# Kernel optimization log

Measured on AMD Instinct MI355X. Metric: run time of the kernel, lower is better.

## Reference

```python
import jax, jax.numpy as jnp
import numpy as np

NB, NC, NT = 64, 128, 6
NEURON = (25, 50, 100)
AXIS = 4
EPS = 1e-12


def _offdiag_idx(nc):
    # static [nc, nc-1] column indices of the off-diagonal entries per row
    idx = np.tile(np.arange(nc)[None, :], (nc, 1))
    mask = ~np.eye(nc, dtype=bool)
    return idx[mask].reshape(nc, nc - 1)


def setup_inputs() -> dict:
    key = jax.random.key(0)
    ks = jax.random.split(key, 8)
    P = NT * NT
    coords = jax.random.normal(ks[0], (NB, NC, 3), dtype=jnp.float32)
    atom_types = jax.random.randint(ks[1], (NC,), 0, NT)
    dims = [1] + list(NEURON)
    inp = {"coords": coords, "atom_types": atom_types}
    for i in range(3):
        bound = 1.0 / float(np.sqrt(dims[i]))
        inp[f"W{i+1}"] = jax.random.uniform(ks[2 + 2 * i], (P, dims[i + 1], dims[i]), jnp.float32, -bound, bound)
        inp[f"b{i+1}"] = jax.random.uniform(ks[3 + 2 * i], (P, dims[i + 1]), jnp.float32, -bound, bound)
    return inp


def _channel_dense(x, W, b, channels, res_mode):
    # x: [nb, Ppairs, in]; W[channels]: [Ppairs, out, in] (redundant per-pair gather, as in torch)
    y = jnp.einsum('bpi,poi->bpo', x, W[channels]) + b[channels]
    y = jnp.tanh(y)
    if res_mode == 1:
        y = y + x
    elif res_mode == 2:
        y = y + jnp.concatenate([x, x], axis=-1)
    return y


def _forward(coords, atom_types, W1, b1, W2, b2, W3, b3):
    nb, nc, _ = coords.shape
    idx = jnp.asarray(_offdiag_idx(nc))  # [nc, nc-1], static
    row = jnp.arange(nc)[:, None]

    rij = coords[:, :, None, :] - coords[:, None, :, :]          # [nb,nc,nc,3]
    rij = rij[:, row, idx]                                       # [nb,nc,nc-1,3] off-diagonal
    dij = jnp.linalg.norm(rij, axis=-1)                          # [nb,nc,nc-1]
    dinv = 1.0 / jnp.maximum(dij, EPS)
    loc_env_r = dinv
    loc_env_a = rij * (dinv * dinv)[..., None]                   # [nb,nc,nc-1,3]

    neighbor_types = atom_types[idx]                             # [nc,nc-1]
    channels = (atom_types[:, None] * NT + neighbor_types).reshape(-1)  # [nc*(nc-1)]

    x = loc_env_r.reshape(nb, -1, 1)                             # [nb,P,1]
    y = _channel_dense(x, W1, b1, channels, res_mode=0)          # 1 -> 25
    y = _channel_dense(y, W2, b2, channels, res_mode=2)          # 25 -> 50 (+concat res)
    y = _channel_dense(y, W3, b3, channels, res_mode=2)          # 50 -> 100 (+concat res)

    out = y.reshape(nb, nc, nc - 1, NEURON[-1])                  # [nb,nc,k,100]
    t1 = jnp.einsum('bnka,bnkf->bnaf', loc_env_a, out[..., :AXIS])   # [nb,nc,3,4]
    t2 = jnp.einsum('bnka,bnaf->bnkf', loc_env_a, t1)                # [nb,nc,k,4]
    res = jnp.einsum('bnkg,bnkf->bngf', out, t2)                     # [nb,nc,100,4]
    return res.reshape(nb, nc, -1)


def reference(coords, atom_types, W1, b1, W2, b2, W3, b3):
    return _forward(coords, atom_types, W1, b1, W2, b2, W3, b3)
```

## Files before the change

### kernel.cpp

```cpp
#include <hip/hip_runtime.h>

#define NBATCH 64
#define NCH    128
#define NTYPE  6
#define NK     127
#define N1     25
#define N2     50
#define N3     100
#define NAXIS  4
#define OUTPER 400
#define W2P    28
#define W3P4   52
#define MAXKP  152
#define MAXC4  38

#define R4(M)  M(0) M(1) M(2) M(3)
#define R5(M)  M(0) M(1) M(2) M(3) M(4)
#define R7(M)  M(0) M(1) M(2) M(3) M(4) M(5) M(6)
#define R12(M) M(0) M(1) M(2) M(3) M(4) M(5) M(6) M(7) M(8) M(9) M(10) M(11)
#define R25(M) M(0) M(1) M(2) M(3) M(4) M(5) M(6) M(7) M(8) M(9) M(10) M(11) M(12) \
               M(13) M(14) M(15) M(16) M(17) M(18) M(19) M(20) M(21) M(22) M(23) M(24)
#define R50(M) R25(M) M(25) M(26) M(27) M(28) M(29) M(30) M(31) M(32) M(33) M(34) \
               M(35) M(36) M(37) M(38) M(39) M(40) M(41) M(42) M(43) M(44) M(45) \
               M(46) M(47) M(48) M(49)

__device__ __forceinline__ float tanh_fast(float x) {
    float e = __expf(2.0f * x);
    return 1.0f - 2.0f * __builtin_amdgcn_rcpf(e + 1.0f);
}

__global__ void k_transpose(const float* __restrict__ coords, float* __restrict__ ct) {
    int t = blockIdx.x * blockDim.x + threadIdx.x;
    if (t >= NBATCH * NCH * 3) return;
    int b  = t & (NBATCH - 1);
    int jd = t >> 6;
    int d  = jd % 3;
    int j  = jd / 3;
    ct[t] = coords[(b * NCH + j) * 3 + d];
}

__device__ __forceinline__ void sort_pad(
    const int* __restrict__ types, int n, int* tysh, int* ksp, int* chs, int* aux,
    int tid, int nthr)
{
    for (int t = tid; t < NCH; t += nthr) tysh[t] = types[t];
    __syncthreads();
    if (tid == 0) {
        int cnt[NTYPE], pos[NTYPE];
        for (int t = 0; t < NTYPE; ++t) cnt[t] = 0;
        for (int k = 0; k < NK; ++k) { int j = (k < n) ? k : k + 1; cnt[tysh[j]]++; }
        int c = 0;
        for (int t = 0; t < NTYPE; ++t) {
            pos[t] = c;
            int pc = (cnt[t] + 3) & ~3;
            for (int q = c >> 2; q < (c + pc) >> 2; ++q) chs[q] = t;
            for (int p = c + cnt[t]; p < c + pc; ++p) ksp[p] = -1;
            c += pc;
        }
        aux[0] = c >> 2;
        for (int k = 0; k < NK; ++k) { int j = (k < n) ? k : k + 1; ksp[pos[tysh[j]]++] = k; }
    }
    __syncthreads();
}

__global__ __launch_bounds__(256, 4) void k_mlp(
    const float* __restrict__ ct, const int* __restrict__ types,
    const float* __restrict__ W1, const float* __restrict__ B1,
    const float* __restrict__ W2, const float* __restrict__ B2,
    const float* __restrict__ W3, const float* __restrict__ B3,
    float* __restrict__ t1buf)
{
    __shared__ float w2s[N2 * W2P];
    __shared__ float w3s4[4 * W3P4];
    __shared__ float w1s[N1], b1s[N1], b2s[N2], b3s4[4];
    __shared__ int   ksp[MAXKP];
    __shared__ int   chs[MAXC4];
    __shared__ int   tysh[NCH];
    __shared__ int   aux[1];

    const int n   = blockIdx.x >> 2;
    const int qc  = blockIdx.x & 3;
    const int w   = threadIdx.x >> 6;
    const int b   = threadIdx.x & 63;
    const int tid = threadIdx.x;

    sort_pad(types, n, tysh, ksp, chs, aux, tid, 256);
    const int nch4 = __builtin_amdgcn_readfirstlane(aux[0]);
    const int c_lo = (qc * nch4) >> 2;
    const int c_hi = ((qc + 1) * nch4) >> 2;

    const int tn = __builtin_amdgcn_readfirstlane(tysh[n]);
    const float cx = ct[(n*3+0)*NBATCH + b];
    const float cy = ct[(n*3+1)*NBATCH + b];
    const float cz = ct[(n*3+2)*NBATCH + b];

    float t1a[12];
#define TIN(i) t1a[i] = 0.0f;
    R12(TIN)
#undef TIN

    int prevty = -1;
    for (int kc = c_lo; kc < c_hi; ++kc) {
        const int tj = __builtin_amdgcn_readfirstlane(chs[kc]);
        const int ch = tn * NTYPE + tj;
        if (tj != prevty) {
            __syncthreads();
            for (int idx = tid; idx < N2*N1; idx += 256)
                w2s[(idx / N1) * W2P + (idx % N1)] = W2[ch*(N2*N1) + idx];
            for (int idx = tid; idx < 4*N2; idx += 256)
                w3s4[(idx / N2) * W3P4 + (idx % N2)] = W3[ch*(N3*N2) + idx];
            if (tid < N1) { w1s[tid] = W1[ch*N1+tid]; b1s[tid] = B1[ch*N1+tid]; }
            if (tid < N2) b2s[tid] = B2[ch*N2+tid];
            if (tid < 4)  b3s4[tid] = B3[ch*N3+tid];
            prevty = tj;
            __syncthreads();
        }
        const int sk = __builtin_amdgcn_readfirstlane(ksp[kc*4 + w]);
        if (sk < 0) continue;
        const int j = (sk < n) ? sk : sk + 1;

        const float dx = cx - ct[(j*3+0)*NBATCH + b];
        const float dy = cy - ct[(j*3+1)*NBATCH + b];
        const float dz = cz - ct[(j*3+2)*NBATCH + b];
        const float d2 = dx*dx + dy*dy + dz*dz;
        const float dd = sqrtf(d2);
        const float dinv = __builtin_amdgcn_rcpf(fmaxf(dd, 1e-12f));
        const float di2 = dinv * dinv;
        const float ax = dx * di2, ay = dy * di2, az = dz * di2;

        float y1[N1];
#define L1S(o) y1[o] = tanh_fast(fmaf(dinv, w1s[o], b1s[o]));
        R25(L1S)
#undef L1S

        float zf0 = b3s4[0], zf1 = b3s4[1], zf2 = b3s4[2], zf3 = b3s4[3];
        float r[4];
#define P1Q(o,q) { float4 wq = *(const float4*)&w2s[(o)*W2P + (q)*4]; \
                   z = fmaf(wq.x, y1[(q)*4+0], z); z = fmaf(wq.y, y1[(q)*4+1], z); \
                   z = fmaf(wq.z, y1[(q)*4+2], z); z = fmaf(wq.w, y1[(q)*4+3], z); }
#define MLP2(o) { float z = b2s[o]; \
                  P1Q(o,0) P1Q(o,1) P1Q(o,2) P1Q(o,3) P1Q(o,4) P1Q(o,5) \
                  z = fmaf(w2s[(o)*W2P + 24], y1[24], z); \
                  float y2o = tanh_fast(z) + y1[(o)%N1]; \
                  if ((o) < 4) r[(o)&3] = y2o; \
                  zf0 = fmaf(w3s4[0*W3P4+(o)], y2o, zf0); \
                  zf1 = fmaf(w3s4[1*W3P4+(o)], y2o, zf1); \
                  zf2 = fmaf(w3s4[2*W3P4+(o)], y2o, zf2); \
                  zf3 = fmaf(w3s4[3*W3P4+(o)], y2o, zf3); }
        R50(MLP2)
#undef MLP2
#undef P1Q

#define O4F(f) { float o4 = tanh_fast(f==0?zf0:f==1?zf1:f==2?zf2:zf3) + r[f]; \
        t1a[0+(f)] = fmaf(ax, o4, t1a[0+(f)]); \
        t1a[4+(f)] = fmaf(ay, o4, t1a[4+(f)]); \
        t1a[8+(f)] = fmaf(az, o4, t1a[8+(f)]); }
        O4F(0) O4F(1) O4F(2) O4F(3)
#undef O4F
    }

    float* dst = t1buf + (n * 12) * NBATCH + b;
#define TAT(i) atomicAdd(dst + (i) * NBATCH, t1a[i]);
    R12(TAT)
#undef TAT
}

__global__ __launch_bounds__(1024, 8) void k_res2(
    const float* __restrict__ ct, const int* __restrict__ types,
    const float* __restrict__ W1, const float* __restrict__ B1,
    const float* __restrict__ W2, const float* __restrict__ B2,
    const float* __restrict__ W3, const float* __restrict__ B3,
    const float* __restrict__ t1buf, float* __restrict__ out)
{
    __shared__ float y2t[4 * N2 * NBATCH];
    __shared__ float t2s[4 * NBATCH * NAXIS];
    __shared__ float w2s[N2 * W2P];
    __shared__ float w1s[N1], b1s[N1], b2s[N2];
    __shared__ int   ksp[MAXKP];
    __shared__ int   chs[MAXC4];
    __shared__ int   tysh[NCH];
    __shared__ int   aux[1];

    const int n    = blockIdx.x >> 1;
    const int kh   = blockIdx.x & 1;
    const int w    = threadIdx.x >> 6;
    const int lane = threadIdx.x & 63;
    const int kk2  = w >> 1;
    const int h    = w & 1;
    const int tid  = threadIdx.x;

    sort_pad(types, n, tysh, ksp, chs, aux, tid, 1024);
    const int nch4 = __builtin_amdgcn_readfirstlane(aux[0]);
    const int c_lo = kh ? (nch4 >> 1) : 0;
    const int c_hi = kh ? nch4 : (nch4 >> 1);

    const int tn = __builtin_amdgcn_readfirstlane(tysh[n]);

    float t1r[12];
#define T1L(i) t1r[i] = t1buf[(n*12 + (i))*NBATCH + lane];
    R12(T1L)
#undef T1L

    const int g0 = __builtin_amdgcn_readfirstlane(w * 7);
    int gg[7], rr[7];
#define GGI(gi) gg[gi] = ((g0 + (gi)) < N3) ? (g0 + (gi)) : (N3 - 1); \
                rr[gi] = (gg[gi] >= N2) ? (gg[gi] - N2) : gg[gi];
    R7(GGI)
#undef GGI

    float racc[7][4];
#define RIN(gi) racc[gi][0]=0.f; racc[gi][1]=0.f; racc[gi][2]=0.f; racc[gi][3]=0.f;
    R7(RIN)
#undef RIN

    float b3v[7];
    int prevty = -1;

    for (int kc = c_lo; kc < c_hi; ++kc) {
        const int tj = __builtin_amdgcn_readfirstlane(chs[kc]);
        const int ch = tn * NTYPE + tj;
        if (tj != prevty) {
            for (int idx = tid; idx < N2*N1; idx += 1024)
                w2s[(idx / N1) * W2P + (idx % N1)] = W2[ch*(N2*N1) + idx];
            if (tid < N1) { w1s[tid] = W1[ch*N1+tid]; b1s[tid] = B1[ch*N1+tid]; }
            if (tid < N2) b2s[tid] = B2[ch*N2+tid];
#define B3L(gi) b3v[gi] = B3[ch*N3 + gg[gi]];
            R7(B3L)
#undef B3L
            prevty = tj;
            __syncthreads();
        }
        const int kb = kc * 4;
        if (w < 8) {
            const int sk = __builtin_amdgcn_readfirstlane(ksp[kb + kk2]);
            if (sk >= 0) {
                const int j = (sk < n) ? sk : sk + 1;
                const float dx = ct[(n*3+0)*NBATCH + lane] - ct[(j*3+0)*NBATCH + lane];
                const float dy = ct[(n*3+1)*NBATCH + lane] - ct[(j*3+1)*NBATCH + lane];
                const float dz = ct[(n*3+2)*NBATCH + lane] - ct[(j*3+2)*NBATCH + lane];
                const float d2 = dx*dx + dy*dy + dz*dz;
                const float dd = sqrtf(d2);
                const float dinv = __builtin_amdgcn_rcpf(fmaxf(dd, 1e-12f));

                if (h == 0) {
                    const float di2 = dinv * dinv;
                    const float ax = dx * di2, ay = dy * di2, az = dz * di2;
#define T2W(f) t2s[(kk2*NBATCH + lane)*NAXIS + (f)] = \
                    ax*t1r[f] + ay*t1r[4+(f)] + az*t1r[8+(f)];
                    T2W(0) T2W(1) T2W(2) T2W(3)
#undef T2W
                }

                float y1[N1];
#define L1S(o) y1[o] = tanh_fast(fmaf(dinv, w1s[o], b1s[o]));
                R25(L1S)
#undef L1S
                const int ob = h * N1;
                float* y2w = &y2t[(kk2*N2 + ob)*NBATCH + lane];
#define P1Q(oi,q) { float4 wq = *(const float4*)&w2s[(ob+(oi))*W2P + (q)*4]; \
                    z = fmaf(wq.x, y1[(q)*4+0], z); z = fmaf(wq.y, y1[(q)*4+1], z); \
                    z = fmaf(wq.z, y1[(q)*4+2], z); z = fmaf(wq.w, y1[(q)*4+3], z); }
#define P1S(oi) { float z = b2s[ob+(oi)]; \
                  P1Q(oi,0) P1Q(oi,1) P1Q(oi,2) P1Q(oi,3) P1Q(oi,4) P1Q(oi,5) \
                  z = fmaf(w2s[(ob+(oi))*W2P + 24], y1[24], z); \
                  y2w[(oi)*NBATCH] = tanh_fast(z) + y1[oi]; }
                R25(P1S)
#undef P1S
#undef P1Q
            }
        }
        __syncthreads();
        const float* w3b = W3 + ch * (N3*N2);
        for (int kp = 0; kp < 2; ++kp) {
            const int skA = __builtin_amdgcn_readfirstlane(ksp[kb + kp*2 + 0]);
            const int skB = __builtin_amdgcn_readfirstlane(ksp[kb + kp*2 + 1]);
            if (skA < 0 && skB < 0) continue;
            const float* y2A = &y2t[((kp*2+0)*N2)*NBATCH + lane];
            const float* y2B = &y2t[((kp*2+1)*N2)*NBATCH + lane];
            float zA[7], zB[7];
#define ZIN(gi) zA[gi] = b3v[gi]; zB[gi] = b3v[gi];
            R7(ZIN)
#undef ZIN
            for (int ic = 0; ic < 10; ++ic) {
                const int io = ic * 5;
                float w35[7][5];
#define W35L(gi) w35[gi][0]=w3b[gg[gi]*N2+io+0]; w35[gi][1]=w3b[gg[gi]*N2+io+1]; \
                 w35[gi][2]=w3b[gg[gi]*N2+io+2]; w35[gi][3]=w3b[gg[gi]*N2+io+3]; \
                 w35[gi][4]=w3b[gg[gi]*N2+io+4];
                R7(W35L)
#undef W35L
                if (skA >= 0) {
                    float yv[5];
#define LDA(i) yv[i] = y2A[(io + (i))*NBATCH];
                    R5(LDA)
#undef LDA
#define FA(gi) zA[gi]=fmaf(w35[gi][0],yv[0],zA[gi]); zA[gi]=fmaf(w35[gi][1],yv[1],zA[gi]); \
               zA[gi]=fmaf(w35[gi][2],yv[2],zA[gi]); zA[gi]=fmaf(w35[gi][3],yv[3],zA[gi]); \
               zA[gi]=fmaf(w35[gi][4],yv[4],zA[gi]);
                    R7(FA)
#undef FA
                }
                if (skB >= 0) {
                    float yv[5];
#define LDB(i) yv[i] = y2B[(io + (i))*NBATCH];
                    R5(LDB)
#undef LDB
#define FB(gi) zB[gi]=fmaf(w35[gi][0],yv[0],zB[gi]); zB[gi]=fmaf(w35[gi][1],yv[1],zB[gi]); \
               zB[gi]=fmaf(w35[gi][2],yv[2],zB[gi]); zB[gi]=fmaf(w35[gi][3],yv[3],zB[gi]); \
               zB[gi]=fmaf(w35[gi][4],yv[4],zB[gi]);
                    R7(FB)
#undef FB
                }
            }
            if (skA >= 0) {
                const float4 t2v = *(const float4*)&t2s[((kp*2+0)*NBATCH + lane)*NAXIS];
#define PFA(gi) { float o3 = tanh_fast(zA[gi]) + y2A[rr[gi]*NBATCH]; \
                  racc[gi][0] = fmaf(o3, t2v.x, racc[gi][0]); \
                  racc[gi][1] = fmaf(o3, t2v.y, racc[gi][1]); \
                  racc[gi][2] = fmaf(o3, t2v.z, racc[gi][2]); \
                  racc[gi][3] = fmaf(o3, t2v.w, racc[gi][3]); }
                R7(PFA)
#undef PFA
            }
            if (skB >= 0) {
                const float4 t2v = *(const float4*)&t2s[((kp*2+1)*NBATCH + lane)*NAXIS];
#define PFB(gi) { float o3 = tanh_fast(zB[gi]) + y2B[rr[gi]*NBATCH]; \
                  racc[gi][0] = fmaf(o3, t2v.x, racc[gi][0]); \
                  racc[gi][1] = fmaf(o3, t2v.y, racc[gi][1]); \
                  racc[gi][2] = fmaf(o3, t2v.z, racc[gi][2]); \
                  racc[gi][3] = fmaf(o3, t2v.w, racc[gi][3]); }
                R7(PFB)
#undef PFB
            }
        }
        __syncthreads();
    }

#define PST(gi) if (g0 + (gi) < N3) { \
        float* dp = &out[(lane*NCH + n)*OUTPER + gg[gi]*NAXIS]; \
        atomicAdd(dp + 0, racc[gi][0]); \
        atomicAdd(dp + 1, racc[gi][1]); \
        atomicAdd(dp + 2, racc[gi][2]); \
        atomicAdd(dp + 3, racc[gi][3]); }
    R7(PST)
#undef PST
}

extern "C" void kernel_launch(void* const* d_in, const int* in_sizes, int n_in,
                              void* d_out, int out_size, void* d_ws, size_t ws_size,
                              hipStream_t stream) {
    const float* coords = (const float*)d_in[0];
    const int*   types  = (const int*)d_in[1];
    const float* W1 = (const float*)d_in[2];
    const float* B1 = (const float*)d_in[3];
    const float* W2 = (const float*)d_in[4];
    const float* B2 = (const float*)d_in[5];
    const float* W3 = (const float*)d_in[6];
    const float* B3 = (const float*)d_in[7];
    float* out = (float*)d_out;

    float* t1buf = (float*)d_ws;
    float* ct    = t1buf + NCH * 12 * NBATCH;

    hipMemsetAsync(t1buf, 0, (size_t)NCH * 12 * NBATCH * sizeof(float), stream);
    hipMemsetAsync(out, 0, (size_t)out_size * sizeof(float), stream);

    k_transpose<<<(NBATCH*NCH*3 + 255)/256, 256, 0, stream>>>(coords, ct);
    k_mlp <<<NCH*4, 256, 0, stream>>>(ct, types, W1,B1,W2,B2,W3,B3, t1buf);
    k_res2<<<NCH*2, 1024, 0, stream>>>(ct, types, W1,B1,W2,B2,W3,B3, t1buf, out);
}
```

Baseline: 1.013 ms.

## Split k_res2 output features across blocks, drop LDS weight staging, use row-major y2

k_res2 now launches 4 blocks per atom of 512 threads each. The extra block dimension splits the 100 output features into two halves of 50, so each wave owns 7 features within its half. W1/W2/B1/B2 are read straight from global memory, which removes the LDS staging and the per-type-change barrier. The y2 intermediate moves to a per-lane row-major layout with padded rows so it can be read and written as float4, and absent neighbours are zero-filled so the skip branches go away. The cost is that layer 1 and layer 2 are recomputed in both feature-half blocks, and padded neighbours now do work they previously skipped.

```diff
diff --git a/kernel.cpp b/kernel.cpp
--- a/kernel.cpp
+++ b/kernel.cpp
@@ -11,15 +11,20 @@
 #define OUTPER 400
 #define W2P    28
 #define W3P4   52
+#define Y2ROW  28
 #define MAXKP  152
 #define MAXC4  38
 
 #define R4(M)  M(0) M(1) M(2) M(3)
 #define R5(M)  M(0) M(1) M(2) M(3) M(4)
+#define R6(M)  M(0) M(1) M(2) M(3) M(4) M(5)
 #define R7(M)  M(0) M(1) M(2) M(3) M(4) M(5) M(6)
 #define R12(M) M(0) M(1) M(2) M(3) M(4) M(5) M(6) M(7) M(8) M(9) M(10) M(11)
 #define R25(M) M(0) M(1) M(2) M(3) M(4) M(5) M(6) M(7) M(8) M(9) M(10) M(11) M(12) \
                M(13) M(14) M(15) M(16) M(17) M(18) M(19) M(20) M(21) M(22) M(23) M(24)
+#define R25A(M,a) M(a,0) M(a,1) M(a,2) M(a,3) M(a,4) M(a,5) M(a,6) M(a,7) M(a,8) M(a,9) \
+               M(a,10) M(a,11) M(a,12) M(a,13) M(a,14) M(a,15) M(a,16) M(a,17) M(a,18) \
+               M(a,19) M(a,20) M(a,21) M(a,22) M(a,23) M(a,24)
 #define R50(M) R25(M) M(25) M(26) M(27) M(28) M(29) M(30) M(31) M(32) M(33) M(34) \
                M(35) M(36) M(37) M(38) M(39) M(40) M(41) M(42) M(43) M(44) M(45) \
                M(46) M(47) M(48) M(49)
@@ -165,23 +170,22 @@
 #undef TAT
 }
 
-__global__ __launch_bounds__(1024, 8) void k_res2(
+__global__ __launch_bounds__(512, 4) void k_res2(
     const float* __restrict__ ct, const int* __restrict__ types,
     const float* __restrict__ W1, const float* __restrict__ B1,
     const float* __restrict__ W2, const float* __restrict__ B2,
     const float* __restrict__ W3, const float* __restrict__ B3,
     const float* __restrict__ t1buf, float* __restrict__ out)
 {
-    __shared__ float y2t[4 * N2 * NBATCH];
+    __shared__ float y2t[4 * 2 * NBATCH * Y2ROW];
     __shared__ float t2s[4 * NBATCH * NAXIS];
-    __shared__ float w2s[N2 * W2P];
-    __shared__ float w1s[N1], b1s[N1], b2s[N2];
     __shared__ int   ksp[MAXKP];
     __shared__ int   chs[MAXC4];
     __shared__ int   tysh[NCH];
     __shared__ int   aux[1];
 
-    const int n    = blockIdx.x >> 1;
+    const int n    = blockIdx.x >> 2;
+    const int gh   = (blockIdx.x >> 1) & 1;
     const int kh   = blockIdx.x & 1;
     const int w    = threadIdx.x >> 6;
     const int lane = threadIdx.x & 63;
@@ -189,7 +193,7 @@
     const int h    = w & 1;
     const int tid  = threadIdx.x;
 
-    sort_pad(types, n, tysh, ksp, chs, aux, tid, 1024);
+    sort_pad(types, n, tysh, ksp, chs, aux, tid, 512);
     const int nch4 = __builtin_amdgcn_readfirstlane(aux[0]);
     const int c_lo = kh ? (nch4 >> 1) : 0;
     const int c_hi = kh ? nch4 : (nch4 >> 1);
@@ -202,9 +206,11 @@
 #undef T1L
 
     const int g0 = __builtin_amdgcn_readfirstlane(w * 7);
-    int gg[7], rr[7];
-#define GGI(gi) gg[gi] = ((g0 + (gi)) < N3) ? (g0 + (gi)) : (N3 - 1); \
-                rr[gi] = (gg[gi] >= N2) ? (gg[gi] - N2) : gg[gi];
+    int gg[7], rh[7], ri[7];
+#define GGI(gi) { int gl = ((g0 + (gi)) < N2) ? (g0 + (gi)) : (N2 - 1); \
+                  gg[gi] = gh * N2 + gl; \
+                  rh[gi] = (gl >= N1) ? 1 : 0; \
+                  ri[gi] = gl - rh[gi] * N1; }
     R7(GGI)
 #undef GGI
 
@@ -213,26 +219,16 @@
     R7(RIN)
 #undef RIN
 
-    float b3v[7];
-    int prevty = -1;
-
     for (int kc = c_lo; kc < c_hi; ++kc) {
-        const int tj = __builtin_amdgcn_readfirstlane(chs[kc]);
-        const int ch = tn * NTYPE + tj;
-        if (tj != prevty) {
-            for (int idx = tid; idx < N2*N1; idx += 1024)
-                w2s[(idx / N1) * W2P + (idx % N1)] = W2[ch*(N2*N1) + idx];
-            if (tid < N1) { w1s[tid] = W1[ch*N1+tid]; b1s[tid] = B1[ch*N1+tid]; }
-            if (tid < N2) b2s[tid] = B2[ch*N2+tid];
+        const int ch = tn * NTYPE + __builtin_amdgcn_readfirstlane(chs[kc]);
+        float b3v[7];
 #define B3L(gi) b3v[gi] = B3[ch*N3 + gg[gi]];
-            R7(B3L)
+        R7(B3L)
 #undef B3L
-            prevty = tj;
-            __syncthreads();
-        }
         const int kb = kc * 4;
-        if (w < 8) {
+        {
             const int sk = __builtin_amdgcn_readfirstlane(ksp[kb + kk2]);
+            float* y2w = &y2t[((kk2*2 + h)*NBATCH + lane)*Y2ROW];
             if (sk >= 0) {
                 const int j = (sk < n) ? sk : sk + 1;
                 const float dx = ct[(n*3+0)*NBATCH + lane] - ct[(j*3+0)*NBATCH + lane];
@@ -245,98 +241,105 @@
                 if (h == 0) {
                     const float di2 = dinv * dinv;
                     const float ax = dx * di2, ay = dy * di2, az = dz * di2;
-#define T2W(f) t2s[(kk2*NBATCH + lane)*NAXIS + (f)] = \
-                    ax*t1r[f] + ay*t1r[4+(f)] + az*t1r[8+(f)];
-                    T2W(0) T2W(1) T2W(2) T2W(3)
-#undef T2W
+                    float4 t2v;
+                    t2v.x = ax*t1r[0] + ay*t1r[4]  + az*t1r[8];
+                    t2v.y = ax*t1r[1] + ay*t1r[5]  + az*t1r[9];
+                    t2v.z = ax*t1r[2] + ay*t1r[6]  + az*t1r[10];
+                    t2v.w = ax*t1r[3] + ay*t1r[7]  + az*t1r[11];
+                    *(float4*)&t2s[(kk2*NBATCH + lane)*NAXIS] = t2v;
                 }
 
+                const float* w1r = W1 + ch * N1;
+                const float* b1r = B1 + ch * N1;
                 float y1[N1];
-#define L1S(o) y1[o] = tanh_fast(fmaf(dinv, w1s[o], b1s[o]));
+#define L1S(o) y1[o] = tanh_fast(fmaf(dinv, w1r[o], b1r[o]));
                 R25(L1S)
 #undef L1S
-                const int ob = h * N1;
-                float* y2w = &y2t[(kk2*N2 + ob)*NBATCH + lane];
-#define P1Q(oi,q) { float4 wq = *(const float4*)&w2s[(ob+(oi))*W2P + (q)*4]; \
-                    z = fmaf(wq.x, y1[(q)*4+0], z); z = fmaf(wq.y, y1[(q)*4+1], z); \
-                    z = fmaf(wq.z, y1[(q)*4+2], z); z = fmaf(wq.w, y1[(q)*4+3], z); }
-#define P1S(oi) { float z = b2s[ob+(oi)]; \
-                  P1Q(oi,0) P1Q(oi,1) P1Q(oi,2) P1Q(oi,3) P1Q(oi,4) P1Q(oi,5) \
-                  z = fmaf(w2s[(ob+(oi))*W2P + 24], y1[24], z); \
-                  y2w[(oi)*NBATCH] = tanh_fast(z) + y1[oi]; }
-                R25(P1S)
-#undef P1S
-#undef P1Q
+                const float* w2h = W2 + ch * (N2*N1) + h * (N1*N1);
+                const float* b2h = B2 + ch * N2 + h * N1;
+#define P1I(oi,i) z = fmaf(w2h[(oi)*N1+(i)], y1[i], z);
+#define P1ROW(oi) ({ float z = b2h[oi]; R25A(P1I,oi) tanh_fast(z) + y1[oi]; })
+#define P1QUAD(q) { float4 v; \
+                    v.x = P1ROW((q)*4+0); v.y = P1ROW((q)*4+1); \
+                    v.z = P1ROW((q)*4+2); v.w = P1ROW((q)*4+3); \
+                    *(float4*)&y2w[(q)*4] = v; }
+                R6(P1QUAD)
+                y2w[24] = P1ROW(24);
+#undef P1QUAD
+#undef P1ROW
+#undef P1I
+            } else {
+                const float4 z4 = make_float4(0.f, 0.f, 0.f, 0.f);
+#define ZQ(q) *(float4*)&y2w[(q)*4] = z4;
+                R6(ZQ)
+#undef ZQ
+                y2w[24] = 0.f;
+                if (h == 0) *(float4*)&t2s[(kk2*NBATCH + lane)*NAXIS] = z4;
             }
         }
         __syncthreads();
         const float* w3b = W3 + ch * (N3*N2);
         for (int kp = 0; kp < 2; ++kp) {
-            const int skA = __builtin_amdgcn_readfirstlane(ksp[kb + kp*2 + 0]);
-            const int skB = __builtin_amdgcn_readfirstlane(ksp[kb + kp*2 + 1]);
-            if (skA < 0 && skB < 0) continue;
-            const float* y2A = &y2t[((kp*2+0)*N2)*NBATCH + lane];
-            const float* y2B = &y2t[((kp*2+1)*N2)*NBATCH + lane];
+            const int kkA = kp*2 + 0, kkB = kp*2 + 1;
+            const float* yA0 = &y2t[((kkA*2+0)*NBATCH + lane)*Y2ROW];
+            const float* yA1 = &y2t[((kkA*2+1)*NBATCH + lane)*Y2ROW];
+            const float* yB0 = &y2t[((kkB*2+0)*NBATCH + lane)*Y2ROW];
+            const float* yB1 = &y2t[((kkB*2+1)*NBATCH + lane)*Y2ROW];
             float zA[7], zB[7];
 #define ZIN(gi) zA[gi] = b3v[gi]; zB[gi] = b3v[gi];
             R7(ZIN)
 #undef ZIN
-            for (int ic = 0; ic < 10; ++ic) {
-                const int io = ic * 5;
-                float w35[7][5];
-#define W35L(gi) w35[gi][0]=w3b[gg[gi]*N2+io+0]; w35[gi][1]=w3b[gg[gi]*N2+io+1]; \
-                 w35[gi][2]=w3b[gg[gi]*N2+io+2]; w35[gi][3]=w3b[gg[gi]*N2+io+3]; \
-                 w35[gi][4]=w3b[gg[gi]*N2+io+4];
-                R7(W35L)
-#undef W35L
-                if (skA >= 0) {
-                    float yv[5];
-#define LDA(i) yv[i] = y2A[(io + (i))*NBATCH];
-                    R5(LDA)
-#undef LDA
-#define FA(gi) zA[gi]=fmaf(w35[gi][0],yv[0],zA[gi]); zA[gi]=fmaf(w35[gi][1],yv[1],zA[gi]); \
-               zA[gi]=fmaf(w35[gi][2],yv[2],zA[gi]); zA[gi]=fmaf(w35[gi][3],yv[3],zA[gi]); \
-               zA[gi]=fmaf(w35[gi][4],yv[4],zA[gi]);
-                    R7(FA)
-#undef FA
-                }
-                if (skB >= 0) {
-                    float yv[5];
-#define LDB(i) yv[i] = y2B[(io + (i))*NBATCH];
-                    R5(LDB)
-#undef LDB
-#define FB(gi) zB[gi]=fmaf(w35[gi][0],yv[0],zB[gi]); zB[gi]=fmaf(w35[gi][1],yv[1],zB[gi]); \
-               zB[gi]=fmaf(w35[gi][2],yv[2],zB[gi]); zB[gi]=fmaf(w35[gi][3],yv[3],zB[gi]); \
-               zB[gi]=fmaf(w35[gi][4],yv[4],zB[gi]);
-                    R7(FB)
-#undef FB
-                }
+#define PW(gi) { const float* wr = w3b + gg[gi]*N2 + ioff + q4; \
+                 const float l0 = wr[0], l1 = wr[1], l2 = wr[2], l3 = wr[3]; \
+                 zA[gi] = fmaf(l0,va.x, fmaf(l1,va.y, fmaf(l2,va.z, fmaf(l3,va.w, zA[gi])))); \
+                 zB[gi] = fmaf(l0,vb.x, fmaf(l1,vb.y, fmaf(l2,vb.z, fmaf(l3,vb.w, zB[gi])))); }
+#define PQ(q) { const int q4 = (q)*4; \
+                const float4 va = *(const float4*)&pA[q4]; \
+                const float4 vb = *(const float4*)&pB[q4]; \
+                R7(PW) }
+            {
+                const float* pA = yA0; const float* pB = yB0; const int ioff = 0;
+                R6(PQ)
+                const float ta = pA[24], tb = pB[24];
+#define PT(gi) { const float lw = w3b[gg[gi]*N2 + ioff + 24]; \
+                 zA[gi] = fmaf(lw, ta, zA[gi]); zB[gi] = fmaf(lw, tb, zB[gi]); }
+                R7(PT)
+#undef PT
             }
-            if (skA >= 0) {
-                const float4 t2v = *(const float4*)&t2s[((kp*2+0)*NBATCH + lane)*NAXIS];
-#define PFA(gi) { float o3 = tanh_fast(zA[gi]) + y2A[rr[gi]*NBATCH]; \
-                  racc[gi][0] = fmaf(o3, t2v.x, racc[gi][0]); \
-                  racc[gi][1] = fmaf(o3, t2v.y, racc[gi][1]); \
-                  racc[gi][2] = fmaf(o3, t2v.z, racc[gi][2]); \
-                  racc[gi][3] = fmaf(o3, t2v.w, racc[gi][3]); }
-                R7(PFA)
+            {
+                const float* pA = yA1; const float* pB = yB1; const int ioff = N1;
+                R6(PQ)
+                const float ta = pA[24], tb = pB[24];
+#define PT(gi) { const float lw = w3b[gg[gi]*N2 + ioff + 24]; \
+                 zA[gi] = fmaf(lw, ta, zA[gi]); zB[gi] = fmaf(lw, tb, zB[gi]); }
+                R7(PT)
+#undef PT
+            }
+#undef PQ
+#undef PW
+            const float4 t2vA = *(const float4*)&t2s[(kkA*NBATCH + lane)*NAXIS];
+            const float4 t2vB = *(const float4*)&t2s[(kkB*NBATCH + lane)*NAXIS];
+#define PFA(gi) { const float* rb = rh[gi] ? yA1 : yA0; \
+                  const float o3 = tanh_fast(zA[gi]) + rb[ri[gi]]; \
+                  racc[gi][0] = fmaf(o3, t2vA.x, racc[gi][0]); \
+                  racc[gi][1] = fmaf(o3, t2vA.y, racc[gi][1]); \
+                  racc[gi][2] = fmaf(o3, t2vA.z, racc[gi][2]); \
+                  racc[gi][3] = fmaf(o3, t2vA.w, racc[gi][3]); }
+            R7(PFA)
 #undef PFA
-            }
-            if (skB >= 0) {
-                const float4 t2v = *(const float4*)&t2s[((kp*2+1)*NBATCH + lane)*NAXIS];
-#define PFB(gi) { float o3 = tanh_fast(zB[gi]) + y2B[rr[gi]*NBATCH]; \
-                  racc[gi][0] = fmaf(o3, t2v.x, racc[gi][0]); \
-                  racc[gi][1] = fmaf(o3, t2v.y, racc[gi][1]); \
-                  racc[gi][2] = fmaf(o3, t2v.z, racc[gi][2]); \
-                  racc[gi][3] = fmaf(o3, t2v.w, racc[gi][3]); }
-                R7(PFB)
+#define PFB(gi) { const float* rb = rh[gi] ? yB1 : yB0; \
+                  const float o3 = tanh_fast(zB[gi]) + rb[ri[gi]]; \
+                  racc[gi][0] = fmaf(o3, t2vB.x, racc[gi][0]); \
+                  racc[gi][1] = fmaf(o3, t2vB.y, racc[gi][1]); \
+                  racc[gi][2] = fmaf(o3, t2vB.z, racc[gi][2]); \
+                  racc[gi][3] = fmaf(o3, t2vB.w, racc[gi][3]); }
+            R7(PFB)
 #undef PFB
-            }
         }
         __syncthreads();
     }
 
-#define PST(gi) if (g0 + (gi) < N3) { \
+#define PST(gi) if (g0 + (gi) < N2) { \
         float* dp = &out[(lane*NCH + n)*OUTPER + gg[gi]*NAXIS]; \
         atomicAdd(dp + 0, racc[gi][0]); \
         atomicAdd(dp + 1, racc[gi][1]); \
@@ -367,5 +370,5 @@
 
     k_transpose<<<(NBATCH*NCH*3 + 255)/256, 256, 0, stream>>>(coords, ct);
     k_mlp <<<NCH*4, 256, 0, stream>>>(ct, types, W1,B1,W2,B2,W3,B3, t1buf);
-    k_res2<<<NCH*2, 1024, 0, stream>>>(ct, types, W1,B1,W2,B2,W3,B3, t1buf, out);
-}
+    k_res2<<<NCH*4, 512, 0, stream>>>(ct, types, W1,B1,W2,B2,W3,B3, t1buf, out);
+}
```

New measurement: 1.452 ms. 1.43x slower.
